# Performance work log

Hardware: AMD Instinct MI355X
Metric: run time of the kernel (lower is better)

The kernel has to match this reference:

```python
import jax, jax.numpy as jnp
import numpy as np

N, E, B = 50000, 640000, 4
H, L = 128, 4
NODE_IN, EDGE_IN, COND_IN, NODE_OUT = 12, 4, 10, 3


def _mlp(x, w1, b1, w2, b2):
    # Linear -> ReLU -> Linear
    return jnp.maximum(x @ w1 + b1, 0.0) @ w2 + b2


def setup_inputs() -> dict:
    key = jax.random.key(0)
    keys = iter(jax.random.split(key, 64))

    def p(*shape):
        fan_in = shape[-2] if len(shape) >= 2 else shape[-1]
        return (jax.random.normal(next(keys), shape, jnp.float32) / np.sqrt(fan_in)).astype(jnp.float32)

    inp = {
        "x": jax.random.normal(next(keys), (N, NODE_IN), jnp.float32),
        "edge_index": jax.random.randint(next(keys), (2, E), 0, N),
        "edge_attr": jax.random.normal(next(keys), (E, EDGE_IN), jnp.float32),
        "conditions": jax.random.normal(next(keys), (B, COND_IN), jnp.float32),
        "batch": jnp.sort(jax.random.randint(next(keys), (N,), 0, B)),
        # encoders
        "enc_node_w1": p(NODE_IN, H), "enc_node_b1": jnp.zeros((H,), jnp.float32),
        "enc_node_w2": p(H, H), "enc_node_b2": jnp.zeros((H,), jnp.float32),
        "enc_edge_w1": p(EDGE_IN, H), "enc_edge_b1": jnp.zeros((H,), jnp.float32),
        "enc_edge_w2": p(H, H), "enc_edge_b2": jnp.zeros((H,), jnp.float32),
        "enc_cond_w1": p(COND_IN, H), "enc_cond_b1": jnp.zeros((H,), jnp.float32),
        "enc_cond_w2": p(H, H), "enc_cond_b2": jnp.zeros((H,), jnp.float32),
        # shared MultiheadAttention: with a single key, softmax weight == 1 per head,
        # so output = out_proj(v_proj(kv)); q/k projections cancel exactly (and have
        # identically zero gradient), so only v/out projections are materialized.
        "attn_wv": p(H, H), "attn_bv": jnp.zeros((H,), jnp.float32),
        "attn_wo": p(H, H), "attn_bo": jnp.zeros((H,), jnp.float32),
        # processor layers (stacked over L)
        "pe_w1": p(L, 4 * H, H), "pe_b1": jnp.zeros((L, H), jnp.float32),
        "pe_w2": p(L, H, H), "pe_b2": jnp.zeros((L, H), jnp.float32),
        "pn_w1": p(L, 3 * H, H), "pn_b1": jnp.zeros((L, H), jnp.float32),
        "pn_w2": p(L, H, H), "pn_b2": jnp.zeros((L, H), jnp.float32),
        # decoder
        "dec_w1": p(H, H), "dec_b1": jnp.zeros((H,), jnp.float32),
        "dec_w2": p(H, NODE_OUT), "dec_b2": jnp.zeros((NODE_OUT,), jnp.float32),
    }
    return inp


def reference(x, edge_index, edge_attr, conditions, batch,
              enc_node_w1, enc_node_b1, enc_node_w2, enc_node_b2,
              enc_edge_w1, enc_edge_b1, enc_edge_w2, enc_edge_b2,
              enc_cond_w1, enc_cond_b1, enc_cond_w2, enc_cond_b2,
              attn_wv, attn_bv, attn_wo, attn_bo,
              pe_w1, pe_b1, pe_w2, pe_b2,
              pn_w1, pn_b1, pn_w2, pn_b2,
              dec_w1, dec_b1, dec_w2, dec_b2):
    n = x.shape[0]
    h = _mlp(x, enc_node_w1, enc_node_b1, enc_node_w2, enc_node_b2)           # [N,H]
    e = _mlp(edge_attr, enc_edge_w1, enc_edge_b1, enc_edge_w2, enc_edge_b2)   # [E,H]
    u = _mlp(conditions, enc_cond_w1, enc_cond_b1, enc_cond_w2, enc_cond_b2)  # [B,H]

    row, col = edge_index[0], edge_index[1]
    u_nodes = u[batch]                                                        # [N,H]
    # single-key cross-attention -> softmax over 1 key == 1 -> out_proj(v_proj(u))
    x_cond = (u_nodes @ attn_wv + attn_bv) @ attn_wo + attn_bo               # [N,H], same every layer
    u_edges = u_nodes[row]                                                    # u[batch[row]]

    for l in range(pe_w1.shape[0]):
        # edge update: cat([src, dest, edge_attr, u[batch_e]]) -> MLP
        e = _mlp(jnp.concatenate([h[row], h[col], e, u_edges], axis=1),
                 pe_w1[l], pe_b1[l], pe_w2[l], pe_b2[l])
        # scatter-add aggregation (index_add on row)
        agg = jax.ops.segment_sum(e, row, num_segments=n)                     # [N,H]
        # node update with residual
        h = h + _mlp(jnp.concatenate([h, agg, x_cond], axis=1),
                     pn_w1[l], pn_b1[l], pn_w2[l], pn_b2[l])

    return _mlp(h, dec_w1, dec_b1, dec_w2, dec_b2)                            # [N,node_out]
```

## Files before the change

kernel.cpp:

```cpp
#include <hip/hip_runtime.h>
#include <cstddef>

#define NN 50000
#define NNP 50048
#define NE 640000
#define NB 4
#define H  128
#define NL 4
#define TE 64

typedef unsigned int u32;
typedef unsigned short u16;
typedef __attribute__((ext_vector_type(8))) short bf16x8;
typedef __attribute__((ext_vector_type(4))) float f32x4;

__device__ __forceinline__ float bf2f(u16 s) {
    union { u32 u; float f; } v; v.u = ((u32)s) << 16; return v.f;
}
__device__ __forceinline__ u16 f2bf(float f) {
    union { float f; u32 u; } v; v.f = f;
    u32 u = v.u;
    u += 0x7FFF + ((u >> 16) & 1);
    return (u16)(u >> 16);
}
__device__ __forceinline__ void unpack8(uint4 raw, float* d) {
    d[0] = bf2f(raw.x & 0xFFFF); d[1] = bf2f(raw.x >> 16);
    d[2] = bf2f(raw.y & 0xFFFF); d[3] = bf2f(raw.y >> 16);
    d[4] = bf2f(raw.z & 0xFFFF); d[5] = bf2f(raw.z >> 16);
    d[6] = bf2f(raw.w & 0xFFFF); d[7] = bf2f(raw.w >> 16);
}
__device__ __forceinline__ bf16x8 ld_f32_bf8(const float* __restrict__ p) {
    const float4 a = *(const float4*)p;
    const float4 b = *(const float4*)(p + 4);
    bf16x8 r;
    r[0] = (short)f2bf(a.x); r[1] = (short)f2bf(a.y);
    r[2] = (short)f2bf(a.z); r[3] = (short)f2bf(a.w);
    r[4] = (short)f2bf(b.x); r[5] = (short)f2bf(b.y);
    r[6] = (short)f2bf(b.z); r[7] = (short)f2bf(b.w);
    return r;
}

__global__ __launch_bounds__(256) void k_zero(float* __restrict__ p, int n4) {
    const int i = blockIdx.x * 256 + threadIdx.x;
    if (i < n4) ((float4*)p)[i] = make_float4(0.f, 0.f, 0.f, 0.f);
}

__global__ __launch_bounds__(256) void k_hist(const int* __restrict__ rowi,
                                              u32* __restrict__ cnt) {
    const int i = blockIdx.x * 256 + threadIdx.x;
    if (i < NE) atomicAdd(&cnt[rowi[i]], 1u);
}

__global__ __launch_bounds__(1024) void k_scan(u32* __restrict__ cnt) {
    __shared__ u32 part[1024];
    const int t = threadIdx.x;
    const int CHUNK = (NN + 1023) / 1024;
    const int lo = t * CHUNK;
    const int hi = (lo + CHUNK < NN) ? lo + CHUNK : NN;
    u32 s = 0;
    for (int i = lo; i < hi; ++i) s += cnt[i];
    part[t] = s;
    __syncthreads();
    for (int ofs = 1; ofs < 1024; ofs <<= 1) {
        const u32 v = (t >= ofs) ? part[t - ofs] : 0u;
        __syncthreads();
        part[t] += v;
        __syncthreads();
    }
    u32 run = (t == 0) ? 0u : part[t - 1];
    for (int i = lo; i < hi; ++i) { const u32 c = cnt[i]; cnt[i] = run; run += c; }
}

__global__ __launch_bounds__(256) void k_scatter(const int* __restrict__ rowi,
                                                 u32* __restrict__ off,
                                                 int* __restrict__ permS) {
    const int i = blockIdx.x * 256 + threadIdx.x;
    if (i < NE) {
        const u32 p = atomicAdd(&off[rowi[i]], 1u);
        permS[p] = i;
    }
}

__global__ __launch_bounds__(256) void k_prep(
    const float* __restrict__ pe_w1, const float* __restrict__ pe_w2,
    const float* __restrict__ pn_w1, const float* __restrict__ pn_w2,
    const float* __restrict__ ew2,   const float* __restrict__ nw2,
    const float* __restrict__ dw1,
    u16* __restrict__ W1t, u16* __restrict__ W2t,
    u16* __restrict__ WaT, u16* __restrict__ WbT,
    u16* __restrict__ Wn1aT, u16* __restrict__ Wn1bT, u16* __restrict__ Wn2T,
    u16* __restrict__ W2et, u16* __restrict__ W2nt, u16* __restrict__ W1dt) {
    const int li = blockIdx.x;
    const float* src; u16* dst;
    switch (blockIdx.y) {
        case 0: src = pe_w1 + ((size_t)li * 512 + 256) * H; dst = W1t  + (size_t)li * H * H; break;
        case 1: src = pe_w2 + (size_t)li * H * H;           dst = W2t  + (size_t)li * H * H; break;
        case 2: src = pe_w1 + (size_t)li * 512 * H;         dst = WaT  + (size_t)li * H * H; break;
        case 3: src = pe_w1 + ((size_t)li * 512 + 128) * H; dst = WbT  + (size_t)li * H * H; break;
        case 4: src = pn_w1 + (size_t)li * 384 * H;         dst = Wn1aT + (size_t)li * H * H; break;
        case 5: src = pn_w1 + ((size_t)li * 384 + 128) * H; dst = Wn1bT + (size_t)li * H * H; break;
        case 6: src = pn_w2 + (size_t)li * H * H;           dst = Wn2T + (size_t)li * H * H; break;
        default:
            if (li == 0)      { src = ew2; dst = W2et; }
            else if (li == 1) { src = nw2; dst = W2nt; }
            else if (li == 2) { src = dw1; dst = W1dt; }
            else return;
            break;
    }
    for (int idx = threadIdx.x; idx < H * H; idx += 256) {
        const int n = idx >> 7, k = idx & 127;
        dst[idx] = f2bf(src[(size_t)k * H + n]);
    }
}

__global__ __launch_bounds__(128) void k_small(
    const float* __restrict__ cond,
    const float* __restrict__ ecw1, const float* __restrict__ ecb1,
    const float* __restrict__ ecw2, const float* __restrict__ ecb2,
    const float* __restrict__ wv, const float* __restrict__ bv,
    const float* __restrict__ wo, const float* __restrict__ bo,
    const float* __restrict__ pe_w1, const float* __restrict__ pe_b1,
    const float* __restrict__ pn_w1, const float* __restrict__ pn_b1,
    float* __restrict__ cbat, float* __restrict__ nbat) {
    __shared__ float tmp[NB][H];
    __shared__ float uL[NB][H];
    __shared__ float xcL[NB][H];
    const int t = threadIdx.x;
    for (int b = 0; b < NB; ++b) {
        float a = ecb1[t];
        for (int k = 0; k < 10; ++k) a = fmaf(cond[b * 10 + k], ecw1[k * H + t], a);
        tmp[b][t] = fmaxf(a, 0.f);
    }
    __syncthreads();
    for (int b = 0; b < NB; ++b) {
        float a = ecb2[t];
        for (int k = 0; k < H; ++k) a = fmaf(tmp[b][k], ecw2[k * H + t], a);
        uL[b][t] = a;
    }
    __syncthreads();
    for (int b = 0; b < NB; ++b) {
        float a = bv[t];
        for (int k = 0; k < H; ++k) a = fmaf(uL[b][k], wv[k * H + t], a);
        tmp[b][t] = a;
    }
    __syncthreads();
    for (int b = 0; b < NB; ++b) {
        float a = bo[t];
        for (int k = 0; k < H; ++k) a = fmaf(tmp[b][k], wo[k * H + t], a);
        xcL[b][t] = a;
    }
    __syncthreads();
    for (int l = 0; l < NL; ++l) {
        const float* w1u = pe_w1 + ((size_t)l * 512 + 384) * H;
        for (int b = 0; b < NB; ++b) {
            float a = pe_b1[l * H + t];
            for (int k = 0; k < H; ++k) a = fmaf(uL[b][k], w1u[k * H + t], a);
            cbat[(l * NB + b) * H + t] = a;
        }
        const float* w1x = pn_w1 + ((size_t)l * 384 + 256) * H;
        for (int b = 0; b < NB; ++b) {
            float a = pn_b1[l * H + t];
            for (int k = 0; k < H; ++k) a = fmaf(xcL[b][k], w1x[k * H + t], a);
            nbat[(l * NB + b) * H + t] = a;
        }
    }
}

__global__ __launch_bounds__(256) void k_enc_e_mfma(
    const float* __restrict__ ea,
    const int* __restrict__ permS,
    const float* __restrict__ w1, const float* __restrict__ b1,
    const u16* __restrict__ W2et, const float* __restrict__ b2,
    u16* __restrict__ e) {
    __shared__ float SI[TE][H + 4];
    const int t = threadIdx.x;
    const long long e0 = (long long)blockIdx.x * TE;
    const int w = t >> 6, l = t & 63;
    const int m16 = l & 15, g = l >> 4;
    const int row = w * 16 + m16;

    const int src = permS[e0 + row];
    const float4 av = *(const float4*)&ea[(size_t)src * 4];

    bf16x8 afrag[4];
#pragma unroll
    for (int ks = 0; ks < 4; ++ks) {
        const int c0 = ks * 32 + g * 8;
        float hv[8];
        {
            const float4 ba = *(const float4*)&b1[c0];
            const float4 bb = *(const float4*)&b1[c0 + 4];
            hv[0] = ba.x; hv[1] = ba.y; hv[2] = ba.z; hv[3] = ba.w;
            hv[4] = bb.x; hv[5] = bb.y; hv[6] = bb.z; hv[7] = bb.w;
        }
#pragma unroll
        for (int k = 0; k < 4; ++k) {
            const float s = (k == 0) ? av.x : (k == 1) ? av.y : (k == 2) ? av.z : av.w;
            const float4 wa = *(const float4*)&w1[k * H + c0];
            const float4 wb = *(const float4*)&w1[k * H + c0 + 4];
            hv[0] = fmaf(s, wa.x, hv[0]); hv[1] = fmaf(s, wa.y, hv[1]);
            hv[2] = fmaf(s, wa.z, hv[2]); hv[3] = fmaf(s, wa.w, hv[3]);
            hv[4] = fmaf(s, wb.x, hv[4]); hv[5] = fmaf(s, wb.y, hv[5]);
            hv[6] = fmaf(s, wb.z, hv[6]); hv[7] = fmaf(s, wb.w, hv[7]);
        }
#pragma unroll
        for (int j = 0; j < 8; ++j) afrag[ks][j] = (short)f2bf(fmaxf(hv[j], 0.f));
    }

    f32x4 acc[8];
#pragma unroll
    for (int nt = 0; nt < 8; ++nt) {
        const float bb = b2[nt * 16 + m16];
        acc[nt][0] = bb; acc[nt][1] = bb; acc[nt][2] = bb; acc[nt][3] = bb;
    }
#pragma unroll
    for (int ks = 0; ks < 4; ++ks) {
#pragma unroll
        for (int nt = 0; nt < 8; ++nt) {
            const bf16x8 bfr =
                *(const bf16x8*)&W2et[(size_t)(nt * 16 + m16) * H + ks * 32 + g * 8];
            acc[nt] = __builtin_amdgcn_mfma_f32_16x16x32_bf16(afrag[ks], bfr, acc[nt], 0, 0, 0);
        }
    }

#pragma unroll
    for (int nt = 0; nt < 8; ++nt)
#pragma unroll
        for (int j = 0; j < 4; ++j)
            SI[w * 16 + g * 4 + j][nt * 16 + m16] = acc[nt][j];
    __syncthreads();
    for (int u = t; u < TE * 16; u += 256) {
        const int j = u >> 4, c8 = (u & 15) * 8;
        const float* sp = &SI[j][c8];
        uint4 pk;
        pk.x = (u32)f2bf(sp[0]) | ((u32)f2bf(sp[1]) << 16);
        pk.y = (u32)f2bf(sp[2]) | ((u32)f2bf(sp[3]) << 16);
        pk.z = (u32)f2bf(sp[4]) | ((u32)f2bf(sp[5]) << 16);
        pk.w = (u32)f2bf(sp[6]) | ((u32)f2bf(sp[7]) << 16);
        *(uint4*)&e[(size_t)(e0 + j) * H + c8] = pk;
    }
}

__global__ __launch_bounds__(256) void k_enc_n_mfma(
    const float* __restrict__ x,
    const float* __restrict__ w1, const float* __restrict__ b1,
    const u16* __restrict__ W2nt, const float* __restrict__ b2,
    float* __restrict__ h) {
    __shared__ float SI[TE][H + 4];
    const int t = threadIdx.x;
    const long long n0 = (long long)blockIdx.x * TE;
    const int w = t >> 6, l = t & 63;
    const int m16 = l & 15, g = l >> 4;
    const int row = w * 16 + m16;
    const long long nr = (n0 + row < NN) ? (n0 + row) : (NN - 1);

    float av[12];
    {
        const float4 a0 = *(const float4*)&x[nr * 12];
        const float4 a1 = *(const float4*)&x[nr * 12 + 4];
        const float4 a2 = *(const float4*)&x[nr * 12 + 8];
        av[0] = a0.x; av[1] = a0.y; av[2] = a0.z; av[3] = a0.w;
        av[4] = a1.x; av[5] = a1.y; av[6] = a1.z; av[7] = a1.w;
        av[8] = a2.x; av[9] = a2.y; av[10] = a2.z; av[11] = a2.w;
    }

    bf16x8 afrag[4];
#pragma unroll
    for (int ks = 0; ks < 4; ++ks) {
        const int c0 = ks * 32 + g * 8;
        float hv[8];
        {
            const float4 ba = *(const float4*)&b1[c0];
            const float4 bb = *(const float4*)&b1[c0 + 4];
            hv[0] = ba.x; hv[1] = ba.y; hv[2] = ba.z; hv[3] = ba.w;
            hv[4] = bb.x; hv[5] = bb.y; hv[6] = bb.z; hv[7] = bb.w;
        }
#pragma unroll
        for (int k = 0; k < 12; ++k) {
            const float s = av[k];
            const float4 wa = *(const float4*)&w1[k * H + c0];
            const float4 wb = *(const float4*)&w1[k * H + c0 + 4];
            hv[0] = fmaf(s, wa.x, hv[0]); hv[1] = fmaf(s, wa.y, hv[1]);
            hv[2] = fmaf(s, wa.z, hv[2]); hv[3] = fmaf(s, wa.w, hv[3]);
            hv[4] = fmaf(s, wb.x, hv[4]); hv[5] = fmaf(s, wb.y, hv[5]);
            hv[6] = fmaf(s, wb.z, hv[6]); hv[7] = fmaf(s, wb.w, hv[7]);
        }
#pragma unroll
        for (int j = 0; j < 8; ++j) afrag[ks][j] = (short)f2bf(fmaxf(hv[j], 0.f));
    }

    f32x4 acc[8];
#pragma unroll
    for (int nt = 0; nt < 8; ++nt) {
        const float bb = b2[nt * 16 + m16];
        acc[nt][0] = bb; acc[nt][1] = bb; acc[nt][2] = bb; acc[nt][3] = bb;
    }
#pragma unroll
    for (int ks = 0; ks < 4; ++ks) {
#pragma unroll
        for (int nt = 0; nt < 8; ++nt) {
            const bf16x8 bfr =
                *(const bf16x8*)&W2nt[(size_t)(nt * 16 + m16) * H + ks * 32 + g * 8];
            acc[nt] = __builtin_amdgcn_mfma_f32_16x16x32_bf16(afrag[ks], bfr, acc[nt], 0, 0, 0);
        }
    }

#pragma unroll
    for (int nt = 0; nt < 8; ++nt)
#pragma unroll
        for (int j = 0; j < 4; ++j)
            SI[w * 16 + g * 4 + j][nt * 16 + m16] = acc[nt][j];
    __syncthreads();
    for (int u = t; u < TE * H / 4; u += 256) {
        const int j = u >> 5, c4 = (u & 31) * 4;
        *(float4*)&h[(size_t)(n0 + j) * H + c4] = *(const float4*)&SI[j][c4];
    }
}

__global__ __launch_bounds__(256) void k_gemm_dual_mfma(
    const float* __restrict__ h,
    const u16* __restrict__ WaT, const u16* __restrict__ WbT,
    u16* __restrict__ Ca, u16* __restrict__ Cb) {
    __shared__ float SI[TE][H + 4];
    const int t = threadIdx.x;
    const long long n0 = (long long)blockIdx.x * TE;
    const int w = t >> 6, l = t & 63;
    const int m16 = l & 15, g = l >> 4;
    const int row = w * 16 + m16;

    bf16x8 afrag[4];
    {
        const float* hp = h + (size_t)(n0 + row) * H + g * 8;
#pragma unroll
        for (int ks = 0; ks < 4; ++ks) afrag[ks] = ld_f32_bf8(hp + ks * 32);
    }

    f32x4 accA[8], accB[8];
#pragma unroll
    for (int nt = 0; nt < 8; ++nt) {
        accA[nt][0] = 0.f; accA[nt][1] = 0.f; accA[nt][2] = 0.f; accA[nt][3] = 0.f;
        accB[nt][0] = 0.f; accB[nt][1] = 0.f; accB[nt][2] = 0.f; accB[nt][3] = 0.f;
    }
#pragma unroll
    for (int ks = 0; ks < 4; ++ks) {
#pragma unroll
        for (int nt = 0; nt < 8; ++nt) {
            const size_t off = (size_t)(nt * 16 + m16) * H + ks * 32 + g * 8;
            const bf16x8 ba = *(const bf16x8*)&WaT[off];
            const bf16x8 bb = *(const bf16x8*)&WbT[off];
            accA[nt] = __builtin_amdgcn_mfma_f32_16x16x32_bf16(afrag[ks], ba, accA[nt], 0, 0, 0);
            accB[nt] = __builtin_amdgcn_mfma_f32_16x16x32_bf16(afrag[ks], bb, accB[nt], 0, 0, 0);
        }
    }

#pragma unroll
    for (int s = 0; s < 2; ++s) {
        __syncthreads();
#pragma unroll
        for (int nt = 0; nt < 8; ++nt)
#pragma unroll
            for (int j = 0; j < 4; ++j)
                SI[w * 16 + g * 4 + j][nt * 16 + m16] = s ? accB[nt][j] : accA[nt][j];
        __syncthreads();
        u16* C = s ? Cb : Ca;
        for (int u = t; u < TE * 16; u += 256) {
            const int j = u >> 4, c8 = (u & 15) * 8;
            const float* sp = &SI[j][c8];
            uint4 pk;
            pk.x = (u32)f2bf(sp[0]) | ((u32)f2bf(sp[1]) << 16);
            pk.y = (u32)f2bf(sp[2]) | ((u32)f2bf(sp[3]) << 16);
            pk.z = (u32)f2bf(sp[4]) | ((u32)f2bf(sp[5]) << 16);
            pk.w = (u32)f2bf(sp[6]) | ((u32)f2bf(sp[7]) << 16);
            *(uint4*)&C[(size_t)(n0 + j) * H + c8] = pk;
        }
    }
}

template <bool WRITE_E>
__global__ __launch_bounds__(256) void k_edge_mfma(
    const u16* __restrict__ hA, const u16* __restrict__ hB,
    const float* __restrict__ cbatl,
    const u16* __restrict__ W1t, const u16* __restrict__ W2t,
    const float* __restrict__ b2,
    const int* __restrict__ rowi, const int* __restrict__ coli,
    const int* __restrict__ batch, const int* __restrict__ permS,
    u16* __restrict__ e, float* __restrict__ agg) {
    __shared__ float SI[TE][H + 4];
    __shared__ int rL[TE], cL[TE], bL[TE];
    const int t = threadIdx.x;
    const long long e0 = (long long)blockIdx.x * TE;

    if (t < TE) {
        const int p = permS[e0 + t];
        const int r = rowi[p];
        rL[t] = r; cL[t] = coli[p]; bL[t] = batch[r];
    }
    __syncthreads();

    for (int u = t; u < TE * 16; u += 256) {
        const int j = u >> 4, c8 = (u & 15) * 8;
        float va[8], vb[8];
        unpack8(*(const uint4*)&hA[(size_t)rL[j] * H + c8], va);
        unpack8(*(const uint4*)&hB[(size_t)cL[j] * H + c8], vb);
        const float* cb = &cbatl[bL[j] * H + c8];
#pragma unroll
        for (int q = 0; q < 8; ++q) SI[j][c8 + q] = va[q] + vb[q] + cb[q];
    }

    const int w = t >> 6, l = t & 63;
    const int m16 = l & 15, g = l >> 4;

    bf16x8 afrag[4];
    {
        const u16* ep = e + (size_t)(e0 + w * 16 + m16) * H + g * 8;
#pragma unroll
        for (int ks = 0; ks < 4; ++ks) afrag[ks] = *(const bf16x8*)(ep + ks * 32);
    }
    __syncthreads();

    f32x4 acc[8];
#pragma unroll
    for (int nt = 0; nt < 8; ++nt) {
#pragma unroll
        for (int j = 0; j < 4; ++j)
            acc[nt][j] = SI[w * 16 + g * 4 + j][nt * 16 + m16];
#pragma unroll
        for (int ks = 0; ks < 4; ++ks) {
            const bf16x8 bfr =
                *(const bf16x8*)&W1t[(size_t)(nt * 16 + m16) * H + ks * 32 + g * 8];
            acc[nt] = __builtin_amdgcn_mfma_f32_16x16x32_bf16(afrag[ks], bfr, acc[nt], 0, 0, 0);
        }
    }
    __syncthreads();

#pragma unroll
    for (int nt = 0; nt < 8; ++nt)
#pragma unroll
        for (int j = 0; j < 4; ++j)
            SI[w * 16 + g * 4 + j][nt * 16 + m16] = fmaxf(acc[nt][j], 0.f);
    __syncthreads();

    f32x4 acc2[8];
#pragma unroll
    for (int nt = 0; nt < 8; ++nt) {
        const float bb = b2[nt * 16 + m16];
        acc2[nt][0] = bb; acc2[nt][1] = bb; acc2[nt][2] = bb; acc2[nt][3] = bb;
    }
#pragma unroll
    for (int ks = 0; ks < 4; ++ks) {
        bf16x8 a2;
        const float* hp = &SI[w * 16 + m16][ks * 32 + g * 8];
#pragma unroll
        for (int j = 0; j < 8; ++j) a2[j] = (short)f2bf(hp[j]);
#pragma unroll
        for (int nt = 0; nt < 8; ++nt) {
            const bf16x8 bfr =
                *(const bf16x8*)&W2t[(size_t)(nt * 16 + m16) * H + ks * 32 + g * 8];
            acc2[nt] = __builtin_amdgcn_mfma_f32_16x16x32_bf16(a2, bfr, acc2[nt], 0, 0, 0);
        }
    }
    __syncthreads();

#pragma unroll
    for (int nt = 0; nt < 8; ++nt)
#pragma unroll
        for (int j = 0; j < 4; ++j)
            SI[w * 16 + g * 4 + j][nt * 16 + m16] = acc2[nt][j];
    __syncthreads();

    if (WRITE_E) {
        for (int u = t; u < TE * 16; u += 256) {
            const int j = u >> 4, c8 = (u & 15) * 8;
            const float* sp = &SI[j][c8];
            uint4 pk;
            pk.x = (u32)f2bf(sp[0]) | ((u32)f2bf(sp[1]) << 16);
            pk.y = (u32)f2bf(sp[2]) | ((u32)f2bf(sp[3]) << 16);
            pk.z = (u32)f2bf(sp[4]) | ((u32)f2bf(sp[5]) << 16);
            pk.w = (u32)f2bf(sp[6]) | ((u32)f2bf(sp[7]) << 16);
            *(uint4*)&e[(size_t)(e0 + j) * H + c8] = pk;
        }
    }

    {
        const int c = t & 127;
        const int j0 = (t >> 7) * 32;
        float sum = SI[j0][c];
        int prev = rL[j0];
        for (int j = j0 + 1; j < j0 + 32; ++j) {
            const int r = rL[j];
            if (r != prev) {
                atomicAdd(&agg[(size_t)prev * H + c], sum);
                sum = 0.f; prev = r;
            }
            sum += SI[j][c];
        }
        atomicAdd(&agg[(size_t)prev * H + c], sum);
    }
}

__global__ __launch_bounds__(256) void k_node_mfma(
    const u16* __restrict__ Wn1aT, const u16* __restrict__ Wn1bT,
    const u16* __restrict__ Wn2T, const float* __restrict__ bn2,
    const float* __restrict__ nbatl, const int* __restrict__ batch,
    const float* __restrict__ agg, float* __restrict__ h) {
    __shared__ float SI[TE][H + 4];
    __shared__ float NBl[NB][H];
    __shared__ int bL[TE];
    const int t = threadIdx.x;
    const long long n0 = (long long)blockIdx.x * TE;
    if (t < TE) {
        const long long n = n0 + t;
        bL[t] = batch[n < NN ? n : (NN - 1)];
    }
    for (int i = t; i < NB * H; i += 256) ((float*)NBl)[i] = nbatl[i];

    const int w = t >> 6, l = t & 63;
    const int m16 = l & 15, g = l >> 4;
    const int row = w * 16 + m16;

    bf16x8 afrag[4];
    {
        const float* hp = h + (size_t)(n0 + row) * H + g * 8;
#pragma unroll
        for (int ks = 0; ks < 4; ++ks) afrag[ks] = ld_f32_bf8(hp + ks * 32);
    }
    __syncthreads();

    f32x4 acc[8];
#pragma unroll
    for (int nt = 0; nt < 8; ++nt)
#pragma unroll
        for (int j = 0; j < 4; ++j)
            acc[nt][j] = NBl[bL[w * 16 + g * 4 + j]][nt * 16 + m16];

#pragma unroll
    for (int ks = 0; ks < 4; ++ks)
#pragma unroll
        for (int nt = 0; nt < 8; ++nt) {
            const bf16x8 bfr =
                *(const bf16x8*)&Wn1aT[(size_t)(nt * 16 + m16) * H + ks * 32 + g * 8];
            acc[nt] = __builtin_amdgcn_mfma_f32_16x16x32_bf16(afrag[ks], bfr, acc[nt], 0, 0, 0);
        }

    {
        const float* ap = agg + (size_t)(n0 + row) * H + g * 8;
#pragma unroll
        for (int ks = 0; ks < 4; ++ks) afrag[ks] = ld_f32_bf8(ap + ks * 32);
    }
#pragma unroll
    for (int ks = 0; ks < 4; ++ks)
#pragma unroll
        for (int nt = 0; nt < 8; ++nt) {
            const bf16x8 bfr =
                *(const bf16x8*)&Wn1bT[(size_t)(nt * 16 + m16) * H + ks * 32 + g * 8];
            acc[nt] = __builtin_amdgcn_mfma_f32_16x16x32_bf16(afrag[ks], bfr, acc[nt], 0, 0, 0);
        }

#pragma unroll
    for (int nt = 0; nt < 8; ++nt)
#pragma unroll
        for (int j = 0; j < 4; ++j)
            SI[w * 16 + g * 4 + j][nt * 16 + m16] = fmaxf(acc[nt][j], 0.f);
    __syncthreads();

    f32x4 acc2[8];
#pragma unroll
    for (int nt = 0; nt < 8; ++nt) {
        const float bb = bn2[nt * 16 + m16];
        acc2[nt][0] = bb; acc2[nt][1] = bb; acc2[nt][2] = bb; acc2[nt][3] = bb;
    }
#pragma unroll
    for (int ks = 0; ks < 4; ++ks) {
        bf16x8 a2;
        const float* hp = &SI[w * 16 + m16][ks * 32 + g * 8];
#pragma unroll
        for (int j = 0; j < 8; ++j) a2[j] = (short)f2bf(hp[j]);
#pragma unroll
        for (int nt = 0; nt < 8; ++nt) {
            const bf16x8 bfr =
                *(const bf16x8*)&Wn2T[(size_t)(nt * 16 + m16) * H + ks * 32 + g * 8];
            acc2[nt] = __builtin_amdgcn_mfma_f32_16x16x32_bf16(a2, bfr, acc2[nt], 0, 0, 0);
        }
    }
    __syncthreads();

#pragma unroll
    for (int nt = 0; nt < 8; ++nt)
#pragma unroll
        for (int j = 0; j < 4; ++j)
            SI[w * 16 + g * 4 + j][nt * 16 + m16] = acc2[nt][j];
    __syncthreads();

    for (int u = t; u < TE * H / 4; u += 256) {
        const int j = u >> 5, c4 = (u & 31) * 4;
        float4 hv = *(const float4*)&h[(size_t)(n0 + j) * H + c4];
        const float4 sv = *(const float4*)&SI[j][c4];
        hv.x += sv.x; hv.y += sv.y; hv.z += sv.z; hv.w += sv.w;
        *(float4*)&h[(size_t)(n0 + j) * H + c4] = hv;
    }
}

__global__ __launch_bounds__(256) void k_dec_mfma(
    const float* __restrict__ h,
    const u16* __restrict__ W1dt, const float* __restrict__ b1,
    const float* __restrict__ w2, const float* __restrict__ b2,
    float* __restrict__ out) {
    __shared__ float SI[TE][H + 4];
    const int t = threadIdx.x;
    const long long n0 = (long long)blockIdx.x * TE;
    const int w = t >> 6, l = t & 63;
    const int m16 = l & 15, g = l >> 4;
    const int row = w * 16 + m16;

    bf16x8 afrag[4];
    {
        const float* hp = h + (size_t)(n0 + row) * H + g * 8;
#pragma unroll
        for (int ks = 0; ks < 4; ++ks) afrag[ks] = ld_f32_bf8(hp + ks * 32);
    }

    f32x4 acc[8];
#pragma unroll
    for (int nt = 0; nt < 8; ++nt) {
        const float bb = b1[nt * 16 + m16];
        acc[nt][0] = bb; acc[nt][1] = bb; acc[nt][2] = bb; acc[nt][3] = bb;
    }
#pragma unroll
    for (int ks = 0; ks < 4; ++ks) {
#pragma unroll
        for (int nt = 0; nt < 8; ++nt) {
            const bf16x8 bfr =
                *(const bf16x8*)&W1dt[(size_t)(nt * 16 + m16) * H + ks * 32 + g * 8];
            acc[nt] = __builtin_amdgcn_mfma_f32_16x16x32_bf16(afrag[ks], bfr, acc[nt], 0, 0, 0);
        }
    }

#pragma unroll
    for (int nt = 0; nt < 8; ++nt)
#pragma unroll
        for (int j = 0; j < 4; ++j)
            SI[w * 16 + g * 4 + j][nt * 16 + m16] = fmaxf(acc[nt][j], 0.f);
    __syncthreads();

    if (t < TE * 3) {
        const int n = t / 3, c = t - n * 3;
        if (n0 + n < NN) {
            float v = b2[c];
            for (int k = 0; k < H; ++k) v = fmaf(SI[n][k], w2[k * 3 + c], v);
            out[(size_t)(n0 + n) * 3 + c] = v;
        }
    }
}

extern "C" void kernel_launch(void* const* d_in, const int* in_sizes, int n_in,
                              void* d_out, int out_size, void* d_ws, size_t ws_size,
                              hipStream_t stream) {
    const float* x          = (const float*)d_in[0];
    const int*   edge_index = (const int*)d_in[1];
    const float* edge_attr  = (const float*)d_in[2];
    const float* cond       = (const float*)d_in[3];
    const int*   batch      = (const int*)d_in[4];
    const float* enc_node_w1 = (const float*)d_in[5];
    const float* enc_node_b1 = (const float*)d_in[6];
    const float* enc_node_w2 = (const float*)d_in[7];
    const float* enc_node_b2 = (const float*)d_in[8];
    const float* enc_edge_w1 = (const float*)d_in[9];
    const float* enc_edge_b1 = (const float*)d_in[10];
    const float* enc_edge_w2 = (const float*)d_in[11];
    const float* enc_edge_b2 = (const float*)d_in[12];
    const float* enc_cond_w1 = (const float*)d_in[13];
    const float* enc_cond_b1 = (const float*)d_in[14];
    const float* enc_cond_w2 = (const float*)d_in[15];
    const float* enc_cond_b2 = (const float*)d_in[16];
    const float* attn_wv = (const float*)d_in[17];
    const float* attn_bv = (const float*)d_in[18];
    const float* attn_wo = (const float*)d_in[19];
    const float* attn_bo = (const float*)d_in[20];
    const float* pe_w1 = (const float*)d_in[21];
    const float* pe_b1 = (const float*)d_in[22];
    const float* pe_w2 = (const float*)d_in[23];
    const float* pe_b2 = (const float*)d_in[24];
    const float* pn_w1 = (const float*)d_in[25];
    const float* pn_b1 = (const float*)d_in[26];
    const float* pn_w2 = (const float*)d_in[27];
    const float* pn_b2 = (const float*)d_in[28];
    const float* dec_w1 = (const float*)d_in[29];
    const float* dec_b1 = (const float*)d_in[30];
    const float* dec_w2 = (const float*)d_in[31];
    const float* dec_b2 = (const float*)d_in[32];

    u16*   e    = (u16*)d_ws;
    float* h    = (float*)((char*)d_ws + (size_t)NE * H * 2);
    float* agg  = h + (size_t)NNP * H;
    u16*   hA   = (u16*)(agg + (size_t)NNP * H);
    u16*   hB   = hA + (size_t)NNP * H;
    float* cbat = (float*)(hB + (size_t)NNP * H);
    float* nbat = cbat + NL * NB * H;
    u16*   W1t   = (u16*)(nbat + NL * NB * H);
    u16*   W2t   = W1t  + (size_t)NL * H * H;
    u16*   WaT   = W2t  + (size_t)NL * H * H;
    u16*   WbT   = WaT  + (size_t)NL * H * H;
    u16*   Wn1aT = WbT  + (size_t)NL * H * H;
    u16*   Wn1bT = Wn1aT + (size_t)NL * H * H;
    u16*   Wn2T  = Wn1bT + (size_t)NL * H * H;
    u16*   W2et  = Wn2T + (size_t)NL * H * H;
    u16*   W2nt  = W2et + (size_t)H * H;
    u16*   W1dt  = W2nt + (size_t)H * H;
    u32*   cnt   = (u32*)(W1dt + (size_t)H * H);
    int*   permS = (int*)(cnt + NNP);

    const int* rowi = edge_index;
    const int* coli = edge_index + NE;
    float* out = (float*)d_out;

    k_zero<<<(NNP / 4 + 255) / 256, 256, 0, stream>>>((float*)cnt, NNP / 4);
    k_hist<<<NE / 256, 256, 0, stream>>>(rowi, cnt);
    k_scan<<<1, 1024, 0, stream>>>(cnt);
    k_scatter<<<NE / 256, 256, 0, stream>>>(rowi, cnt, permS);

    k_prep<<<dim3(NL, 8), 256, 0, stream>>>(pe_w1, pe_w2, pn_w1, pn_w2,
                                            enc_edge_w2, enc_node_w2, dec_w1,
                                            W1t, W2t, WaT, WbT,
                                            Wn1aT, Wn1bT, Wn2T, W2et, W2nt, W1dt);
    k_small<<<1, 128, 0, stream>>>(cond, enc_cond_w1, enc_cond_b1, enc_cond_w2, enc_cond_b2,
                                   attn_wv, attn_bv, attn_wo, attn_bo,
                                   pe_w1, pe_b1, pn_w1, pn_b1, cbat, nbat);
    k_enc_n_mfma<<<NNP / TE, 256, 0, stream>>>(
        x, enc_node_w1, enc_node_b1, W2nt, enc_node_b2, h);
    k_enc_e_mfma<<<NE / TE, 256, 0, stream>>>(
        edge_attr, permS, enc_edge_w1, enc_edge_b1, W2et, enc_edge_b2, e);

    for (int l = 0; l < NL; ++l) {
        k_zero<<<(NNP * H / 4 + 255) / 256, 256, 0, stream>>>(agg, NNP * H / 4);
        k_gemm_dual_mfma<<<NNP / TE, 256, 0, stream>>>(h, WaT + (size_t)l * H * H,
                                                       WbT + (size_t)l * H * H, hA, hB);
        if (l < NL - 1)
            k_edge_mfma<true><<<NE / TE, 256, 0, stream>>>(
                hA, hB, cbat + l * NB * H,
                W1t + (size_t)l * H * H, W2t + (size_t)l * H * H,
                pe_b2 + l * H, rowi, coli, batch, permS, e, agg);
        else
            k_edge_mfma<false><<<NE / TE, 256, 0, stream>>>(
                hA, hB, cbat + l * NB * H,
                W1t + (size_t)l * H * H, W2t + (size_t)l * H * H,
                pe_b2 + l * H, rowi, coli, batch, permS, e, agg);
        k_node_mfma<<<NNP / TE, 256, 0, stream>>>(
            Wn1aT + (size_t)l * H * H, Wn1bT + (size_t)l * H * H,
            Wn2T + (size_t)l * H * H, pn_b2 + l * H,
            nbat + l * NB * H, batch, agg, h);
    }
    k_dec_mfma<<<NNP / TE, 256, 0, stream>>>(h, W1dt, dec_b1, dec_w2, dec_b2, out);
}
```

Before: 2.485 ms.

## Pre-sort edge indices, use bf16 LDS staging, aggregate from registers

Result: slower. 2.607 ms (+4.9%).

```diff
diff --git a/kernel.cpp b/kernel.cpp
--- a/kernel.cpp
+++ b/kernel.cpp
@@ -28,6 +28,14 @@
     d[2] = bf2f(raw.y & 0xFFFF); d[3] = bf2f(raw.y >> 16);
     d[4] = bf2f(raw.z & 0xFFFF); d[5] = bf2f(raw.z >> 16);
     d[6] = bf2f(raw.w & 0xFFFF); d[7] = bf2f(raw.w >> 16);
+}
+__device__ __forceinline__ uint4 pack8(const float* s) {
+    uint4 pk;
+    pk.x = (u32)f2bf(s[0]) | ((u32)f2bf(s[1]) << 16);
+    pk.y = (u32)f2bf(s[2]) | ((u32)f2bf(s[3]) << 16);
+    pk.z = (u32)f2bf(s[4]) | ((u32)f2bf(s[5]) << 16);
+    pk.w = (u32)f2bf(s[6]) | ((u32)f2bf(s[7]) << 16);
+    return pk;
 }
 __device__ __forceinline__ bf16x8 ld_f32_bf8(const float* __restrict__ p) {
     const float4 a = *(const float4*)p;
@@ -72,12 +80,16 @@
 }
 
 __global__ __launch_bounds__(256) void k_scatter(const int* __restrict__ rowi,
+                                                 const int* __restrict__ coli,
                                                  u32* __restrict__ off,
-                                                 int* __restrict__ permS) {
+                                                 int* __restrict__ permS,
+                                                 int* __restrict__ rowS,
+                                                 int* __restrict__ colS) {
     const int i = blockIdx.x * 256 + threadIdx.x;
     if (i < NE) {
-        const u32 p = atomicAdd(&off[rowi[i]], 1u);
-        permS[p] = i;
+        const int r = rowi[i];
+        const u32 p = atomicAdd(&off[r], 1u);
+        permS[p] = i; rowS[p] = r; colS[p] = coli[i];
     }
 }
 
@@ -231,13 +243,7 @@
     __syncthreads();
     for (int u = t; u < TE * 16; u += 256) {
         const int j = u >> 4, c8 = (u & 15) * 8;
-        const float* sp = &SI[j][c8];
-        uint4 pk;
-        pk.x = (u32)f2bf(sp[0]) | ((u32)f2bf(sp[1]) << 16);
-        pk.y = (u32)f2bf(sp[2]) | ((u32)f2bf(sp[3]) << 16);
-        pk.z = (u32)f2bf(sp[4]) | ((u32)f2bf(sp[5]) << 16);
-        pk.w = (u32)f2bf(sp[6]) | ((u32)f2bf(sp[7]) << 16);
-        *(uint4*)&e[(size_t)(e0 + j) * H + c8] = pk;
+        *(uint4*)&e[(size_t)(e0 + j) * H + c8] = pack8(&SI[j][c8]);
     }
 }
 
@@ -321,7 +327,7 @@
     const float* __restrict__ h,
     const u16* __restrict__ WaT, const u16* __restrict__ WbT,
     u16* __restrict__ Ca, u16* __restrict__ Cb) {
-    __shared__ float SI[TE][H + 4];
+    __shared__ u16 SI[TE][H + 8];
     const int t = threadIdx.x;
     const long long n0 = (long long)blockIdx.x * TE;
     const int w = t >> 6, l = t & 63;
@@ -360,18 +366,13 @@
         for (int nt = 0; nt < 8; ++nt)
 #pragma unroll
             for (int j = 0; j < 4; ++j)
-                SI[w * 16 + g * 4 + j][nt * 16 + m16] = s ? accB[nt][j] : accA[nt][j];
+                SI[w * 16 + g * 4 + j][nt * 16 + m16] =
+                    f2bf(s ? accB[nt][j] : accA[nt][j]);
         __syncthreads();
         u16* C = s ? Cb : Ca;
         for (int u = t; u < TE * 16; u += 256) {
             const int j = u >> 4, c8 = (u & 15) * 8;
-            const float* sp = &SI[j][c8];
-            uint4 pk;
-            pk.x = (u32)f2bf(sp[0]) | ((u32)f2bf(sp[1]) << 16);
-            pk.y = (u32)f2bf(sp[2]) | ((u32)f2bf(sp[3]) << 16);
-            pk.z = (u32)f2bf(sp[4]) | ((u32)f2bf(sp[5]) << 16);
-            pk.w = (u32)f2bf(sp[6]) | ((u32)f2bf(sp[7]) << 16);
-            *(uint4*)&C[(size_t)(n0 + j) * H + c8] = pk;
+            *(uint4*)&C[(size_t)(n0 + j) * H + c8] = *(const uint4*)&SI[j][c8];
         }
     }
 }
@@ -382,39 +383,38 @@
     const float* __restrict__ cbatl,
     const u16* __restrict__ W1t, const u16* __restrict__ W2t,
     const float* __restrict__ b2,
-    const int* __restrict__ rowi, const int* __restrict__ coli,
-    const int* __restrict__ batch, const int* __restrict__ permS,
+    const int* __restrict__ rowS, const int* __restrict__ colS,
+    const int* __restrict__ batch,
     u16* __restrict__ e, float* __restrict__ agg) {
-    __shared__ float SI[TE][H + 4];
+    __shared__ u16 SI[TE][H + 8];
     __shared__ int rL[TE], cL[TE], bL[TE];
     const int t = threadIdx.x;
     const long long e0 = (long long)blockIdx.x * TE;
+    const int w = t >> 6, l = t & 63;
+    const int m16 = l & 15, g = l >> 4;
+
+    bf16x8 afrag[4];
+    {
+        const u16* ep = e + (size_t)(e0 + w * 16 + m16) * H + g * 8;
+#pragma unroll
+        for (int ks = 0; ks < 4; ++ks) afrag[ks] = *(const bf16x8*)(ep + ks * 32);
+    }
 
     if (t < TE) {
-        const int p = permS[e0 + t];
-        const int r = rowi[p];
-        rL[t] = r; cL[t] = coli[p]; bL[t] = batch[r];
+        const int r = rowS[e0 + t];
+        rL[t] = r; cL[t] = colS[e0 + t]; bL[t] = batch[r];
     }
     __syncthreads();
 
     for (int u = t; u < TE * 16; u += 256) {
         const int j = u >> 4, c8 = (u & 15) * 8;
-        float va[8], vb[8];
+        float va[8], vb[8], sm[8];
         unpack8(*(const uint4*)&hA[(size_t)rL[j] * H + c8], va);
         unpack8(*(const uint4*)&hB[(size_t)cL[j] * H + c8], vb);
         const float* cb = &cbatl[bL[j] * H + c8];
 #pragma unroll
-        for (int q = 0; q < 8; ++q) SI[j][c8 + q] = va[q] + vb[q] + cb[q];
-    }
-
-    const int w = t >> 6, l = t & 63;
-    const int m16 = l & 15, g = l >> 4;
-
-    bf16x8 afrag[4];
-    {
-        const u16* ep = e + (size_t)(e0 + w * 16 + m16) * H + g * 8;
-#pragma unroll
-        for (int ks = 0; ks < 4; ++ks) afrag[ks] = *(const bf16x8*)(ep + ks * 32);
+        for (int q = 0; q < 8; ++q) sm[q] = va[q] + vb[q] + cb[q];
+        *(uint4*)&SI[j][c8] = pack8(sm);
     }
     __syncthreads();
 
@@ -423,7 +423,7 @@
     for (int nt = 0; nt < 8; ++nt) {
 #pragma unroll
         for (int j = 0; j < 4; ++j)
-            acc[nt][j] = SI[w * 16 + g * 4 + j][nt * 16 + m16];
+            acc[nt][j] = bf2f(SI[w * 16 + g * 4 + j][nt * 16 + m16]);
 #pragma unroll
         for (int ks = 0; ks < 4; ++ks) {
             const bf16x8 bfr =
@@ -437,7 +437,7 @@
     for (int nt = 0; nt < 8; ++nt)
 #pragma unroll
         for (int j = 0; j < 4; ++j)
-            SI[w * 16 + g * 4 + j][nt * 16 + m16] = fmaxf(acc[nt][j], 0.f);
+            SI[w * 16 + g * 4 + j][nt * 16 + m16] = f2bf(fmaxf(acc[nt][j], 0.f));
     __syncthreads();
 
     f32x4 acc2[8];
@@ -448,10 +448,7 @@
     }
 #pragma unroll
     for (int ks = 0; ks < 4; ++ks) {
-        bf16x8 a2;
-        const float* hp = &SI[w * 16 + m16][ks * 32 + g * 8];
-#pragma unroll
-        for (int j = 0; j < 8; ++j) a2[j] = (short)f2bf(hp[j]);
+        const bf16x8 a2 = *(const bf16x8*)&SI[w * 16 + m16][ks * 32 + g * 8];
 #pragma unroll
         for (int nt = 0; nt < 8; ++nt) {
             const bf16x8 bfr =
@@ -459,42 +456,37 @@
             acc2[nt] = __builtin_amdgcn_mfma_f32_16x16x32_bf16(a2, bfr, acc2[nt], 0, 0, 0);
         }
     }
-    __syncthreads();
-
-#pragma unroll
-    for (int nt = 0; nt < 8; ++nt)
-#pragma unroll
-        for (int j = 0; j < 4; ++j)
-            SI[w * 16 + g * 4 + j][nt * 16 + m16] = acc2[nt][j];
-    __syncthreads();
 
     if (WRITE_E) {
+        __syncthreads();
+#pragma unroll
+        for (int nt = 0; nt < 8; ++nt)
+#pragma unroll
+            for (int j = 0; j < 4; ++j)
+                SI[w * 16 + g * 4 + j][nt * 16 + m16] = f2bf(acc2[nt][j]);
+        __syncthreads();
         for (int u = t; u < TE * 16; u += 256) {
             const int j = u >> 4, c8 = (u & 15) * 8;
-            const float* sp = &SI[j][c8];
-            uint4 pk;
-            pk.x = (u32)f2bf(sp[0]) | ((u32)f2bf(sp[1]) << 16);
-            pk.y = (u32)f2bf(sp[2]) | ((u32)f2bf(sp[3]) << 16);
-            pk.z = (u32)f2bf(sp[4]) | ((u32)f2bf(sp[5]) << 16);
-            pk.w = (u32)f2bf(sp[6]) | ((u32)f2bf(sp[7]) << 16);
-            *(uint4*)&e[(size_t)(e0 + j) * H + c8] = pk;
+            *(uint4*)&e[(size_t)(e0 + j) * H + c8] = *(const uint4*)&SI[j][c8];
         }
     }
 
     {
-        const int c = t & 127;
-        const int j0 = (t >> 7) * 32;
-        float sum = SI[j0][c];
-        int prev = rL[j0];
-        for (int j = j0 + 1; j < j0 + 32; ++j) {
-            const int r = rL[j];
-            if (r != prev) {
-                atomicAdd(&agg[(size_t)prev * H + c], sum);
-                sum = 0.f; prev = r;
-            }
-            sum += SI[j][c];
-        }
-        atomicAdd(&agg[(size_t)prev * H + c], sum);
+        const int base = w * 16 + g * 4;
+        const int r0 = rL[base], r1 = rL[base + 1], r2 = rL[base + 2], r3 = rL[base + 3];
+#pragma unroll
+        for (int nt = 0; nt < 8; ++nt) {
+            const int c = nt * 16 + m16;
+            float s = acc2[nt][0];
+            int prev = r0;
+            if (r1 == prev) s += acc2[nt][1];
+            else { atomicAdd(&agg[(size_t)prev * H + c], s); s = acc2[nt][1]; prev = r1; }
+            if (r2 == prev) s += acc2[nt][2];
+            else { atomicAdd(&agg[(size_t)prev * H + c], s); s = acc2[nt][2]; prev = r2; }
+            if (r3 == prev) s += acc2[nt][3];
+            else { atomicAdd(&agg[(size_t)prev * H + c], s); s = acc2[nt][3]; prev = r3; }
+            atomicAdd(&agg[(size_t)prev * H + c], s);
+        }
     }
 }
 
@@ -708,6 +700,8 @@
     u16*   W1dt  = W2nt + (size_t)H * H;
     u32*   cnt   = (u32*)(W1dt + (size_t)H * H);
     int*   permS = (int*)(cnt + NNP);
+    int*   rowS  = permS + NE;
+    int*   colS  = rowS + NE;
 
     const int* rowi = edge_index;
     const int* coli = edge_index + NE;
@@ -716,7 +710,7 @@
     k_zero<<<(NNP / 4 + 255) / 256, 256, 0, stream>>>((float*)cnt, NNP / 4);
     k_hist<<<NE / 256, 256, 0, stream>>>(rowi, cnt);
     k_scan<<<1, 1024, 0, stream>>>(cnt);
-    k_scatter<<<NE / 256, 256, 0, stream>>>(rowi, cnt, permS);
+    k_scatter<<<NE / 256, 256, 0, stream>>>(rowi, coli, cnt, permS, rowS, colS);
 
     k_prep<<<dim3(NL, 8), 256, 0, stream>>>(pe_w1, pe_w2, pn_w1, pn_w2,
                                             enc_edge_w2, enc_node_w2, dec_w1,
@@ -738,12 +732,12 @@
             k_edge_mfma<true><<<NE / TE, 256, 0, stream>>>(
                 hA, hB, cbat + l * NB * H,
                 W1t + (size_t)l * H * H, W2t + (size_t)l * H * H,
-                pe_b2 + l * H, rowi, coli, batch, permS, e, agg);
+                pe_b2 + l * H, rowS, colS, batch, e, agg);
         else
             k_edge_mfma<false><<<NE / TE, 256, 0, stream>>>(
                 hA, hB, cbat + l * NB * H,
                 W1t + (size_t)l * H * H, W2t + (size_t)l * H * H,
-                pe_b2 + l * H, rowi, coli, batch, permS, e, agg);
+                pe_b2 + l * H, rowS, colS, batch, e, agg);
         k_node_mfma<<<NNP / TE, 256, 0, stream>>>(
             Wn1aT + (size_t)l * H * H, Wn1bT + (size_t)l * H * H,
             Wn2T + (size_t)l * H * H, pn_b2 + l * H,
```
